# Optimization experiments

Measured on AMD Instinct MI355X. Metric: run time of the kernel, lower is better.

## Reference

```python
import jax, jax.numpy as jnp
import numpy as np

ENC_H = 128
DEC_H = 256
DEC_STEPS = 10


def _gru_cell(x, h, Wih, Whh, bih, bhh):
    # PyTorch GRU cell, gate order (r, z, n)
    gi = x @ Wih.T + bih          # (B, 3H)
    gh = h @ Whh.T + bhh          # (B, 3H)
    H = h.shape[-1]
    ir, iz, inn = gi[:, :H], gi[:, H:2 * H], gi[:, 2 * H:]
    hr, hz, hn = gh[:, :H], gh[:, H:2 * H], gh[:, 2 * H:]
    r = jax.nn.sigmoid(ir + hr)
    z = jax.nn.sigmoid(iz + hz)
    n = jnp.tanh(inn + r * hn)
    return (1.0 - z) * n + z * h


def setup_inputs() -> dict:
    key = jax.random.key(0)
    ks = jax.random.split(key, 12)
    B, S = 4096, 128
    s = 0.1
    return {
        "x": jax.random.normal(ks[0], (B, S, 5), jnp.float32),
        "y": jax.random.normal(ks[1], (B, S, 1), jnp.float32),
        "enc_Wih": jax.random.normal(ks[2], (3 * ENC_H, 5), jnp.float32) * s,
        "enc_Whh": jax.random.normal(ks[3], (3 * ENC_H, ENC_H), jnp.float32) * s,
        "enc_bih": jax.random.normal(ks[4], (3 * ENC_H,), jnp.float32) * s,
        "enc_bhh": jax.random.normal(ks[5], (3 * ENC_H,), jnp.float32) * s,
        "dec_Wih": jax.random.normal(ks[6], (3 * DEC_H, ENC_H + 1), jnp.float32) * s,
        "dec_Whh": jax.random.normal(ks[7], (3 * DEC_H, DEC_H), jnp.float32) * s,
        "dec_bih": jax.random.normal(ks[8], (3 * DEC_H,), jnp.float32) * s,
        "dec_bhh": jax.random.normal(ks[9], (3 * DEC_H,), jnp.float32) * s,
        "lin_W": jax.random.normal(ks[10], (4, DEC_H), jnp.float32) * s,
        "lin_b": jax.random.normal(ks[11], (4,), jnp.float32) * s,
    }


def reference(x, y, enc_Wih, enc_Whh, enc_bih, enc_bhh,
              dec_Wih, dec_Whh, dec_bih, dec_bhh, lin_W, lin_b):
    B, S, _ = x.shape
    xs = jnp.transpose(x, (1, 0, 2))   # (S, B, 5)
    ys = jnp.transpose(y, (1, 0, 2))   # (S, B, 1)

    # Encoder: only the final hidden state (contex) is consumed downstream.
    h0 = jnp.zeros((B, ENC_H), x.dtype)

    def enc_step(h, xt):
        return _gru_cell(xt, h, enc_Wih, enc_Whh, enc_bih, enc_bhh), None

    contex, _ = jax.lax.scan(enc_step, h0, xs)   # (B, 128)

    # Decoder: initial hidden is ones (torch.ones_like(shape)), 10 steps.
    hdec0 = jnp.ones((B, DEC_H), x.dtype)

    def dec_step(h, yt):
        xt = jnp.concatenate([contex, yt], axis=-1)   # (B, 129)
        h2 = _gru_cell(xt, h, dec_Wih, dec_Whh, dec_bih, dec_bhh)
        out = h2 @ lin_W.T + lin_b                    # (B, 4)
        return h2, out

    _, outs = jax.lax.scan(dec_step, hdec0, ys[:DEC_STEPS])  # (10, B, 4)

    # res starts as ones; only first 10 rows written.
    res = jnp.ones((S, B, 4), x.dtype).at[:DEC_STEPS].set(outs)
    return jnp.transpose(res, (1, 0, 2))   # (B, S, 4)
```

## Files before the change

### kernel.cpp

```cpp
#include <hip/hip_runtime.h>

#define B_SZ 4096
#define S_SZ 128
#define XD 5
#define EH 128
#define DH 256
#define DSTEPS 10

typedef short v8s __attribute__((ext_vector_type(8)));
typedef float v4f __attribute__((ext_vector_type(4)));

__device__ __forceinline__ float bf2f(unsigned short u) {
    union { unsigned int i; float f; } v; v.i = ((unsigned int)u) << 16; return v.f;
}
__device__ __forceinline__ unsigned short f2bf(float f) {
    union { float f; unsigned int i; } v; v.f = f;
    unsigned int x = v.i;
    return (unsigned short)((x + 0x7FFFu + ((x >> 16) & 1u)) >> 16);
}
__device__ __forceinline__ float fexp2(float x) { return __builtin_amdgcn_exp2f(x); }
__device__ __forceinline__ float frcp(float x) { return __builtin_amdgcn_rcpf(x); }
__device__ __forceinline__ float sigmoidf_(float x) {
    return frcp(1.f + fexp2(-1.44269504088896f * x));
}
__device__ __forceinline__ float tanhf_(float x) {
    float e = fexp2(2.88539008177793f * x);
    return 1.f - 2.f * frcp(e + 1.f);
}

__global__ __launch_bounds__(512) void enc_kernel(
    const float* __restrict__ x,
    const float* __restrict__ Wih32,
    const float* __restrict__ Whh32,
    const float* __restrict__ bih,
    const float* __restrict__ bhh,
    const float* __restrict__ dWih,
    const float* __restrict__ dWhh,
    unsigned short* __restrict__ wihp,
    unsigned short* __restrict__ dWhh_bf,
    unsigned short* __restrict__ ctex)
{
    __shared__ unsigned short xs[S_SZ][16][8];
    __shared__ unsigned short hb[2][16][136];
    __shared__ unsigned short zpad[8];

    const int tid = threadIdx.x;
    const int bid = blockIdx.x;
    const int wv = tid >> 6;
    const int lane = tid & 63;
    const int n = lane & 15;
    const int kg = lane >> 4;
    const int r0 = bid * 16;

    for (int i = bid * 512 + tid; i < 768 * 256; i += 131072)
        dWhh_bf[i] = f2bf(dWhh[i]);
    for (int i = bid * 512 + tid; i < 768 * 136; i += 131072) {
        int col = i / 136, k = i - col * 136;
        wihp[i] = (k < 129) ? f2bf(dWih[col * 129 + k]) : (unsigned short)0;
    }

    for (int i = tid; i < 2 * 16 * 136; i += 512) ((unsigned short*)hb)[i] = 0;
    if (tid < 8) zpad[tid] = 0;
    for (int i = tid; i < 16 * S_SZ * 8; i += 512) {
        int m = i >> 10;
        int rem = i & 1023;
        int t = rem >> 3;
        int j = rem & 7;
        unsigned short v = 0;
        if (j < XD) v = f2bf(x[(size_t)(r0 + m) * (S_SZ * XD) + t * XD + j]);
        xs[t][m][j] = v;
    }

    const int colw = wv * 16 + n;
    v8s fw[3][4];
    v8s fx[3];
    #pragma unroll
    for (int g = 0; g < 3; ++g) {
        int gcol = g * EH + colw;
        #pragma unroll
        for (int kt = 0; kt < 4; ++kt) {
            const float* p = &Whh32[(size_t)gcol * EH + kt * 32 + kg * 8];
            float4 lo = *(const float4*)p;
            float4 hi = *(const float4*)(p + 4);
            v8s f;
            f[0] = (short)f2bf(lo.x); f[1] = (short)f2bf(lo.y);
            f[2] = (short)f2bf(lo.z); f[3] = (short)f2bf(lo.w);
            f[4] = (short)f2bf(hi.x); f[5] = (short)f2bf(hi.y);
            f[6] = (short)f2bf(hi.z); f[7] = (short)f2bf(hi.w);
            fw[g][kt] = f;
        }
        v8s t = {0, 0, 0, 0, 0, 0, 0, 0};
        if (kg == 0) {
            const float* p = &Wih32[gcol * XD];
            #pragma unroll
            for (int j = 0; j < XD; ++j) t[j] = (short)f2bf(p[j]);
        }
        fx[g] = t;
    }
    const float b_r  = bih[colw]          + bhh[colw];
    const float b_z  = bih[EH + colw]     + bhh[EH + colw];
    const float bi_n = bih[2 * EH + colw];
    const float bh_n = bhh[2 * EH + colw];

    float hst[4] = {0.f, 0.f, 0.f, 0.f};
    __syncthreads();

    #pragma unroll 2
    for (int t = 0; t < S_SZ; ++t) {
        const int p = t & 1;
        v8s a[4];
        #pragma unroll
        for (int kt = 0; kt < 4; ++kt)
            a[kt] = *(const v8s*)&hb[p][n][kt * 32 + kg * 8];
        const unsigned short* xsrc = (kg == 0) ? &xs[t][n][0] : &zpad[0];
        v8s ax = *(const v8s*)xsrc;

        v4f accr  = {b_r, b_r, b_r, b_r};
        v4f accz  = {b_z, b_z, b_z, b_z};
        v4f acchn = {bh_n, bh_n, bh_n, bh_n};
        v4f accin = {bi_n, bi_n, bi_n, bi_n};
        #pragma unroll
        for (int kt = 0; kt < 4; ++kt) {
            accr  = __builtin_amdgcn_mfma_f32_16x16x32_bf16(a[kt], fw[0][kt], accr, 0, 0, 0);
            accz  = __builtin_amdgcn_mfma_f32_16x16x32_bf16(a[kt], fw[1][kt], accz, 0, 0, 0);
            acchn = __builtin_amdgcn_mfma_f32_16x16x32_bf16(a[kt], fw[2][kt], acchn, 0, 0, 0);
        }
        accr  = __builtin_amdgcn_mfma_f32_16x16x32_bf16(ax, fx[0], accr, 0, 0, 0);
        accz  = __builtin_amdgcn_mfma_f32_16x16x32_bf16(ax, fx[1], accz, 0, 0, 0);
        accin = __builtin_amdgcn_mfma_f32_16x16x32_bf16(ax, fx[2], accin, 0, 0, 0);

        #pragma unroll
        for (int e = 0; e < 4; ++e) {
            float r = sigmoidf_(accr[e]);
            float z = sigmoidf_(accz[e]);
            float nn = tanhf_(accin[e] + r * acchn[e]);
            float h = (1.f - z) * nn + z * hst[e];
            hst[e] = h;
            hb[1 - p][kg * 4 + e][colw] = f2bf(h);
        }
        __syncthreads();
    }
    #pragma unroll
    for (int e = 0; e < 4; ++e)
        ctex[(size_t)(r0 + kg * 4 + e) * EH + colw] = f2bf(hst[e]);
}

__global__ __launch_bounds__(512)
__attribute__((amdgpu_waves_per_eu(2, 2)))
void dec_all_kernel(
    const unsigned short* __restrict__ dWhh_bf,
    const unsigned short* __restrict__ wihp,
    const float* __restrict__ dbih,
    const float* __restrict__ dbhh,
    const float* __restrict__ y,
    const unsigned short* __restrict__ ctex,
    const float* __restrict__ linW,
    const float* __restrict__ linb,
    float* __restrict__ out)
{
    __shared__ unsigned short wshn[32 * 264 * 8];
    __shared__ unsigned short hshf[32 * 16 * 8];
    __shared__ unsigned short lwf[32 * 16 * 8];

    const int tid  = threadIdx.x;
    const int w    = tid >> 6;
    const int lane = tid & 63;
    const int n    = lane & 15;
    const int kg   = lane >> 4;
    const int rb   = blockIdx.x * 16;
    const int cbase = w * 32;

    for (int i = tid; i < 256 * 32; i += 512) {
        int col = i >> 5, kgrp = i & 31;
        uint4 v = *(const uint4*)&dWhh_bf[(size_t)(512 + col) * 256 + kgrp * 8];
        *(uint4*)&wshn[(kgrp * 264 + col) * 8] = v;
    }
    {
        int col = tid >> 5, kgrp = tid & 31;
        unsigned short v8[8];
        #pragma unroll
        for (int j = 0; j < 8; ++j)
            v8[j] = (col < 4) ? f2bf(linW[col * 256 + kgrp * 8 + j]) : (unsigned short)0;
        *(uint4*)&lwf[(kgrp * 16 + col) * 8] = *(uint4*)v8;
    }
    for (int i = tid; i < 32 * 16 * 8; i += 512) hshf[i] = 0x3F80;

    v8s fB[2][8];
    #pragma unroll
    for (int g = 0; g < 2; ++g)
        #pragma unroll
        for (int kt = 0; kt < 8; ++kt)
            fB[g][kt] = *(const v8s*)
                &dWhh_bf[(size_t)(g * DH + cbase + n) * DH + kt * 32 + kg * 8];
    #pragma unroll
    for (int g = 0; g < 2; ++g)
        #pragma unroll
        for (int kt = 0; kt < 8; ++kt)
            asm volatile("" : "+v"(fB[g][kt]));

    const unsigned short* pR1 = &dWhh_bf[(size_t)(0 * DH + cbase + 16 + n) * DH + kg * 8];
    const unsigned short* pZ1 = &dWhh_bf[(size_t)(1 * DH + cbase + 16 + n) * DH + kg * 8];

    v4f gi[3][2];
    float wy[3][2], bNh[2];
    #pragma unroll
    for (int g = 0; g < 3; ++g)
        #pragma unroll
        for (int cg = 0; cg < 2; ++cg) {
            int gcol = g * DH + cbase + cg * 16 + n;
            float bb = dbih[gcol] + ((g < 2) ? dbhh[gcol] : 0.f);
            gi[g][cg] = (v4f){bb, bb, bb, bb};
            wy[g][cg] = bf2f(wihp[(size_t)gcol * 136 + 128]);
        }
    #pragma unroll
    for (int cg = 0; cg < 2; ++cg)
        bNh[cg] = dbhh[2 * DH + cbase + cg * 16 + n];

    #pragma unroll
    for (int kt = 0; kt < 4; ++kt) {
        v8s a = *(const v8s*)&ctex[(size_t)(rb + n) * EH + kt * 32 + kg * 8];
        #pragma unroll
        for (int g = 0; g < 3; ++g)
            #pragma unroll
            for (int cg = 0; cg < 2; ++cg) {
                v8s b = *(const v8s*)
                    &wihp[(size_t)(g * DH + cbase + cg * 16 + n) * 136 + kt * 32 + kg * 8];
                gi[g][cg] = __builtin_amdgcn_mfma_f32_16x16x32_bf16(a, b, gi[g][cg], 0, 0, 0);
            }
    }

    const float lb = (n < 4) ? linb[n] : 0.f;
    float hprev[2][4];
    #pragma unroll
    for (int cg = 0; cg < 2; ++cg)
        #pragma unroll
        for (int e = 0; e < 4; ++e) hprev[cg][e] = 1.0f;

    __syncthreads();

    #pragma clang loop unroll(disable)
    for (int t = 0; t < DSTEPS; ++t) {
        float yv[4];
        #pragma unroll
        for (int e = 0; e < 4; ++e)
            yv[e] = y[(size_t)(rb + kg * 4 + e) * S_SZ + t];

        v4f ar[2], az[2], an[2];
        #pragma unroll
        for (int cg = 0; cg < 2; ++cg) {
            ar[cg] = (v4f){0.f, 0.f, 0.f, 0.f};
            az[cg] = (v4f){0.f, 0.f, 0.f, 0.f};
            an[cg] = (v4f){bNh[cg], bNh[cg], bNh[cg], bNh[cg]};
        }
        #pragma unroll
        for (int kt = 0; kt < 8; ++kt) {
            v8s a   = *(const v8s*)&hshf[((kt * 4 + kg) * 16 + n) * 8];
            v8s br1 = *(const v8s*)&pR1[kt * 32];
            v8s bz1 = *(const v8s*)&pZ1[kt * 32];
            v8s bn0 = *(const v8s*)&wshn[((kt * 4 + kg) * 264 + cbase + n) * 8];
            v8s bn1 = *(const v8s*)&wshn[((kt * 4 + kg) * 264 + cbase + 16 + n) * 8];
            ar[0] = __builtin_amdgcn_mfma_f32_16x16x32_bf16(a, fB[0][kt], ar[0], 0, 0, 0);
            az[0] = __builtin_amdgcn_mfma_f32_16x16x32_bf16(a, fB[1][kt], az[0], 0, 0, 0);
            an[0] = __builtin_amdgcn_mfma_f32_16x16x32_bf16(a, bn0,      an[0], 0, 0, 0);
            ar[1] = __builtin_amdgcn_mfma_f32_16x16x32_bf16(a, br1,      ar[1], 0, 0, 0);
            az[1] = __builtin_amdgcn_mfma_f32_16x16x32_bf16(a, bz1,      az[1], 0, 0, 0);
            an[1] = __builtin_amdgcn_mfma_f32_16x16x32_bf16(a, bn1,      an[1], 0, 0, 0);
        }
        __syncthreads();

        #pragma unroll
        for (int cg = 0; cg < 2; ++cg) {
            const int chi = 4 * w + 2 * cg + (n >> 3);
            #pragma unroll
            for (int e = 0; e < 4; ++e) {
                float r  = sigmoidf_(gi[0][cg][e] + yv[e] * wy[0][cg] + ar[cg][e]);
                float z  = sigmoidf_(gi[1][cg][e] + yv[e] * wy[1][cg] + az[cg][e]);
                float nn = tanhf_(gi[2][cg][e] + yv[e] * wy[2][cg] + r * an[cg][e]);
                float h  = nn + z * (hprev[cg][e] - nn);
                hprev[cg][e] = h;
                hshf[(chi * 16 + kg * 4 + e) * 8 + (n & 7)] = f2bf(h);
            }
        }
        __syncthreads();

        if (w == 0) {
            v4f o4 = {0.f, 0.f, 0.f, 0.f};
            #pragma unroll
            for (int kt = 0; kt < 8; ++kt) {
                v8s a = *(const v8s*)&hshf[((kt * 4 + kg) * 16 + n) * 8];
                v8s b = *(const v8s*)&lwf[((kt * 4 + kg) * 16 + n) * 8];
                o4 = __builtin_amdgcn_mfma_f32_16x16x32_bf16(a, b, o4, 0, 0, 0);
            }
            if (n < 4) {
                #pragma unroll
                for (int e = 0; e < 4; ++e)
                    out[(size_t)(rb + kg * 4 + e) * (S_SZ * 4) + t * 4 + n] = o4[e] + lb;
            }
        }
    }

    for (int j = tid; j < 16 * 512; j += 512) {
        int row = j >> 9, c = j & 511;
        if (c >= DSTEPS * 4) out[(size_t)(rb + row) * 512 + c] = 1.0f;
    }
}

extern "C" void kernel_launch(void* const* d_in, const int* in_sizes, int n_in,
                              void* d_out, int out_size, void* d_ws, size_t ws_size,
                              hipStream_t stream)
{
    const float* x    = (const float*)d_in[0];
    const float* y    = (const float*)d_in[1];
    const float* eWih = (const float*)d_in[2];
    const float* eWhh = (const float*)d_in[3];
    const float* ebih = (const float*)d_in[4];
    const float* ebhh = (const float*)d_in[5];
    const float* dWih = (const float*)d_in[6];
    const float* dWhh = (const float*)d_in[7];
    const float* dbih = (const float*)d_in[8];
    const float* dbhh = (const float*)d_in[9];
    const float* linW = (const float*)d_in[10];
    const float* linb = (const float*)d_in[11];
    float* out = (float*)d_out;

    char* ws = (char*)d_ws;
    unsigned short* wihp    = (unsigned short*)(ws);
    unsigned short* dWhh_bf = (unsigned short*)(ws + 208896);
    unsigned short* ctex    = (unsigned short*)(ws + 602112);

    enc_kernel<<<256, 512, 0, stream>>>(x, eWih, eWhh, ebih, ebhh,
                                        dWih, dWhh, wihp, dWhh_bf, ctex);
    dec_all_kernel<<<256, 512, 0, stream>>>(dWhh_bf, wihp, dbih, dbhh, y,
                                            ctex, linW, linb, out);
}
```

Baseline: 217.6 us.

## Ping-pong encoder recurrence across two wave groups to overlap MFMA and gates

Splits the encoder block's 8 waves into two groups, each handling 8 of the 16 batch rows with its own hidden-state buffer. Each wave now computes 32 columns. The groups run out of phase: while one group issues MFMAs for its rows, the other evaluates the gate nonlinearities for its rows, separated by two barriers per step. The aim is to hide the serial MFMA-then-activation latency of the recurrence, at the cost of half the MFMA rows being wasted padding, double the per-wave weight registers, and an extra barrier per step.

```diff
diff --git a/kernel.cpp b/kernel.cpp
--- a/kernel.cpp
+++ b/kernel.cpp
@@ -28,7 +28,9 @@
     return 1.f - 2.f * frcp(e + 1.f);
 }
 
-__global__ __launch_bounds__(512) void enc_kernel(
+__global__ __launch_bounds__(512)
+__attribute__((amdgpu_waves_per_eu(2, 2)))
+void enc_kernel(
     const float* __restrict__ x,
     const float* __restrict__ Wih32,
     const float* __restrict__ Whh32,
@@ -41,12 +43,15 @@
     unsigned short* __restrict__ ctex)
 {
     __shared__ unsigned short xs[S_SZ][16][8];
-    __shared__ unsigned short hb[2][16][136];
+    __shared__ unsigned short bufA[2][16][136];
+    __shared__ unsigned short bufB[2][16][136];
     __shared__ unsigned short zpad[8];
 
     const int tid = threadIdx.x;
     const int bid = blockIdx.x;
-    const int wv = tid >> 6;
+    const int w = tid >> 6;
+    const int ws = w & 3;
+    const bool isA = (w < 4);
     const int lane = tid & 63;
     const int n = lane & 15;
     const int kg = lane >> 4;
@@ -59,7 +64,10 @@
         wihp[i] = (k < 129) ? f2bf(dWih[col * 129 + k]) : (unsigned short)0;
     }
 
-    for (int i = tid; i < 2 * 16 * 136; i += 512) ((unsigned short*)hb)[i] = 0;
+    for (int i = tid; i < 2 * 16 * 136; i += 512) {
+        ((unsigned short*)bufA)[i] = 0;
+        ((unsigned short*)bufB)[i] = 0;
+    }
     if (tid < 8) zpad[tid] = 0;
     for (int i = tid; i < 16 * S_SZ * 8; i += 512) {
         int m = i >> 10;
@@ -71,78 +79,161 @@
         xs[t][m][j] = v;
     }
 
-    const int colw = wv * 16 + n;
-    v8s fw[3][4];
-    v8s fx[3];
-    #pragma unroll
-    for (int g = 0; g < 3; ++g) {
-        int gcol = g * EH + colw;
-        #pragma unroll
-        for (int kt = 0; kt < 4; ++kt) {
-            const float* p = &Whh32[(size_t)gcol * EH + kt * 32 + kg * 8];
-            float4 lo = *(const float4*)p;
-            float4 hi = *(const float4*)(p + 4);
-            v8s f;
-            f[0] = (short)f2bf(lo.x); f[1] = (short)f2bf(lo.y);
-            f[2] = (short)f2bf(lo.z); f[3] = (short)f2bf(lo.w);
-            f[4] = (short)f2bf(hi.x); f[5] = (short)f2bf(hi.y);
-            f[6] = (short)f2bf(hi.z); f[7] = (short)f2bf(hi.w);
-            fw[g][kt] = f;
-        }
-        v8s t = {0, 0, 0, 0, 0, 0, 0, 0};
-        if (kg == 0) {
-            const float* p = &Wih32[gcol * XD];
-            #pragma unroll
-            for (int j = 0; j < XD; ++j) t[j] = (short)f2bf(p[j]);
-        }
-        fx[g] = t;
-    }
-    const float b_r  = bih[colw]          + bhh[colw];
-    const float b_z  = bih[EH + colw]     + bhh[EH + colw];
-    const float bi_n = bih[2 * EH + colw];
-    const float bh_n = bhh[2 * EH + colw];
-
-    float hst[4] = {0.f, 0.f, 0.f, 0.f};
+    v8s fw[3][2][4];
+    v8s fx[3][2];
+    float b_r[2], b_z[2], bi_n[2], bh_n[2];
+    #pragma unroll
+    for (int cg = 0; cg < 2; ++cg) {
+        const int colw = ws * 32 + cg * 16 + n;
+        #pragma unroll
+        for (int g = 0; g < 3; ++g) {
+            int gcol = g * EH + colw;
+            #pragma unroll
+            for (int kt = 0; kt < 4; ++kt) {
+                const float* p = &Whh32[(size_t)gcol * EH + kt * 32 + kg * 8];
+                float4 lo = *(const float4*)p;
+                float4 hi = *(const float4*)(p + 4);
+                v8s f;
+                f[0] = (short)f2bf(lo.x); f[1] = (short)f2bf(lo.y);
+                f[2] = (short)f2bf(lo.z); f[3] = (short)f2bf(lo.w);
+                f[4] = (short)f2bf(hi.x); f[5] = (short)f2bf(hi.y);
+                f[6] = (short)f2bf(hi.z); f[7] = (short)f2bf(hi.w);
+                fw[g][cg][kt] = f;
+            }
+            v8s t = {0, 0, 0, 0, 0, 0, 0, 0};
+            if (kg == 0) {
+                const float* p = &Wih32[gcol * XD];
+                #pragma unroll
+                for (int j = 0; j < XD; ++j) t[j] = (short)f2bf(p[j]);
+            }
+            fx[g][cg] = t;
+        }
+        b_r[cg]  = bih[colw]          + bhh[colw];
+        b_z[cg]  = bih[EH + colw]     + bhh[EH + colw];
+        bi_n[cg] = bih[2 * EH + colw];
+        bh_n[cg] = bhh[2 * EH + colw];
+    }
+
+    float hst[2][4] = {{0.f, 0.f, 0.f, 0.f}, {0.f, 0.f, 0.f, 0.f}};
+    v4f accr[2], accz[2], acchn[2], accin[2];
     __syncthreads();
 
-    #pragma unroll 2
-    for (int t = 0; t < S_SZ; ++t) {
-        const int p = t & 1;
-        v8s a[4];
-        #pragma unroll
-        for (int kt = 0; kt < 4; ++kt)
-            a[kt] = *(const v8s*)&hb[p][n][kt * 32 + kg * 8];
-        const unsigned short* xsrc = (kg == 0) ? &xs[t][n][0] : &zpad[0];
-        v8s ax = *(const v8s*)xsrc;
-
-        v4f accr  = {b_r, b_r, b_r, b_r};
-        v4f accz  = {b_z, b_z, b_z, b_z};
-        v4f acchn = {bh_n, bh_n, bh_n, bh_n};
-        v4f accin = {bi_n, bi_n, bi_n, bi_n};
-        #pragma unroll
-        for (int kt = 0; kt < 4; ++kt) {
-            accr  = __builtin_amdgcn_mfma_f32_16x16x32_bf16(a[kt], fw[0][kt], accr, 0, 0, 0);
-            accz  = __builtin_amdgcn_mfma_f32_16x16x32_bf16(a[kt], fw[1][kt], accz, 0, 0, 0);
-            acchn = __builtin_amdgcn_mfma_f32_16x16x32_bf16(a[kt], fw[2][kt], acchn, 0, 0, 0);
-        }
-        accr  = __builtin_amdgcn_mfma_f32_16x16x32_bf16(ax, fx[0], accr, 0, 0, 0);
-        accz  = __builtin_amdgcn_mfma_f32_16x16x32_bf16(ax, fx[1], accz, 0, 0, 0);
-        accin = __builtin_amdgcn_mfma_f32_16x16x32_bf16(ax, fx[2], accin, 0, 0, 0);
-
-        #pragma unroll
-        for (int e = 0; e < 4; ++e) {
-            float r = sigmoidf_(accr[e]);
-            float z = sigmoidf_(accz[e]);
-            float nn = tanhf_(accin[e] + r * acchn[e]);
-            float h = (1.f - z) * nn + z * hst[e];
-            hst[e] = h;
-            hb[1 - p][kg * 4 + e][colw] = f2bf(h);
+    for (int i = 0; i < S_SZ; ++i) {
+        const int p = i & 1;
+        if (isA) {
+            v8s a[4];
+            #pragma unroll
+            for (int kt = 0; kt < 4; ++kt)
+                a[kt] = *(const v8s*)&bufA[p][n][kt * 32 + kg * 8];
+            const unsigned short* xsrc = (kg == 0) ? &xs[i][n][0] : &zpad[0];
+            v8s ax = *(const v8s*)xsrc;
+            #pragma unroll
+            for (int cg = 0; cg < 2; ++cg) {
+                accr[cg]  = (v4f){b_r[cg], b_r[cg], b_r[cg], b_r[cg]};
+                accz[cg]  = (v4f){b_z[cg], b_z[cg], b_z[cg], b_z[cg]};
+                acchn[cg] = (v4f){bh_n[cg], bh_n[cg], bh_n[cg], bh_n[cg]};
+                accin[cg] = (v4f){bi_n[cg], bi_n[cg], bi_n[cg], bi_n[cg]};
+            }
+            #pragma unroll
+            for (int kt = 0; kt < 4; ++kt)
+                #pragma unroll
+                for (int cg = 0; cg < 2; ++cg) {
+                    accr[cg]  = __builtin_amdgcn_mfma_f32_16x16x32_bf16(a[kt], fw[0][cg][kt], accr[cg], 0, 0, 0);
+                    accz[cg]  = __builtin_amdgcn_mfma_f32_16x16x32_bf16(a[kt], fw[1][cg][kt], accz[cg], 0, 0, 0);
+                    acchn[cg] = __builtin_amdgcn_mfma_f32_16x16x32_bf16(a[kt], fw[2][cg][kt], acchn[cg], 0, 0, 0);
+                }
+            #pragma unroll
+            for (int cg = 0; cg < 2; ++cg) {
+                accr[cg]  = __builtin_amdgcn_mfma_f32_16x16x32_bf16(ax, fx[0][cg], accr[cg], 0, 0, 0);
+                accz[cg]  = __builtin_amdgcn_mfma_f32_16x16x32_bf16(ax, fx[1][cg], accz[cg], 0, 0, 0);
+                accin[cg] = __builtin_amdgcn_mfma_f32_16x16x32_bf16(ax, fx[2][cg], accin[cg], 0, 0, 0);
+            }
+        } else if (i > 0) {
+            if (kg < 2) {
+                #pragma unroll
+                for (int cg = 0; cg < 2; ++cg) {
+                    const int colw = ws * 32 + cg * 16 + n;
+                    #pragma unroll
+                    for (int e = 0; e < 4; ++e) {
+                        float r = sigmoidf_(accr[cg][e]);
+                        float z = sigmoidf_(accz[cg][e]);
+                        float nn = tanhf_(accin[cg][e] + r * acchn[cg][e]);
+                        float h = (1.f - z) * nn + z * hst[cg][e];
+                        hst[cg][e] = h;
+                        bufB[p][kg * 4 + e][colw] = f2bf(h);
+                    }
+                }
+            }
         }
         __syncthreads();
-    }
-    #pragma unroll
-    for (int e = 0; e < 4; ++e)
-        ctex[(size_t)(r0 + kg * 4 + e) * EH + colw] = f2bf(hst[e]);
+        if (isA) {
+            if (kg < 2) {
+                #pragma unroll
+                for (int cg = 0; cg < 2; ++cg) {
+                    const int colw = ws * 32 + cg * 16 + n;
+                    #pragma unroll
+                    for (int e = 0; e < 4; ++e) {
+                        float r = sigmoidf_(accr[cg][e]);
+                        float z = sigmoidf_(accz[cg][e]);
+                        float nn = tanhf_(accin[cg][e] + r * acchn[cg][e]);
+                        float h = (1.f - z) * nn + z * hst[cg][e];
+                        hst[cg][e] = h;
+                        bufA[1 - p][kg * 4 + e][colw] = f2bf(h);
+                    }
+                }
+            }
+        } else {
+            v8s a[4];
+            #pragma unroll
+            for (int kt = 0; kt < 4; ++kt)
+                a[kt] = *(const v8s*)&bufB[p][n][kt * 32 + kg * 8];
+            const unsigned short* xsrc = (kg == 0) ? &xs[i][8 + (n & 7)][0] : &zpad[0];
+            v8s ax = *(const v8s*)xsrc;
+            #pragma unroll
+            for (int cg = 0; cg < 2; ++cg) {
+                accr[cg]  = (v4f){b_r[cg], b_r[cg], b_r[cg], b_r[cg]};
+                accz[cg]  = (v4f){b_z[cg], b_z[cg], b_z[cg], b_z[cg]};
+                acchn[cg] = (v4f){bh_n[cg], bh_n[cg], bh_n[cg], bh_n[cg]};
+                accin[cg] = (v4f){bi_n[cg], bi_n[cg], bi_n[cg], bi_n[cg]};
+            }
+            #pragma unroll
+            for (int kt = 0; kt < 4; ++kt)
+                #pragma unroll
+                for (int cg = 0; cg < 2; ++cg) {
+                    accr[cg]  = __builtin_amdgcn_mfma_f32_16x16x32_bf16(a[kt], fw[0][cg][kt], accr[cg], 0, 0, 0);
+                    accz[cg]  = __builtin_amdgcn_mfma_f32_16x16x32_bf16(a[kt], fw[1][cg][kt], accz[cg], 0, 0, 0);
+                    acchn[cg] = __builtin_amdgcn_mfma_f32_16x16x32_bf16(a[kt], fw[2][cg][kt], acchn[cg], 0, 0, 0);
+                }
+            #pragma unroll
+            for (int cg = 0; cg < 2; ++cg) {
+                accr[cg]  = __builtin_amdgcn_mfma_f32_16x16x32_bf16(ax, fx[0][cg], accr[cg], 0, 0, 0);
+                accz[cg]  = __builtin_amdgcn_mfma_f32_16x16x32_bf16(ax, fx[1][cg], accz[cg], 0, 0, 0);
+                accin[cg] = __builtin_amdgcn_mfma_f32_16x16x32_bf16(ax, fx[2][cg], accin[cg], 0, 0, 0);
+            }
+        }
+        __syncthreads();
+    }
+    if (!isA && kg < 2) {
+        #pragma unroll
+        for (int cg = 0; cg < 2; ++cg)
+            #pragma unroll
+            for (int e = 0; e < 4; ++e) {
+                float r = sigmoidf_(accr[cg][e]);
+                float z = sigmoidf_(accz[cg][e]);
+                float nn = tanhf_(accin[cg][e] + r * acchn[cg][e]);
+                hst[cg][e] = nn + z * (hst[cg][e] - nn);
+            }
+    }
+    if (kg < 2) {
+        const int rowoff = isA ? 0 : 8;
+        #pragma unroll
+        for (int cg = 0; cg < 2; ++cg) {
+            const int colw = ws * 32 + cg * 16 + n;
+            #pragma unroll
+            for (int e = 0; e < 4; ++e)
+                ctex[(size_t)(r0 + rowoff + kg * 4 + e) * EH + colw] = f2bf(hst[cg][e]);
+        }
+    }
 }
 
 __global__ __launch_bounds__(512)
```

New measurement: 303.0 us. 39.3% more time.
